# Performance work log

Measured on AMD Instinct MI355X. Metric: run time of the kernel, lower is better.

Reference implementation:

```python
import jax, jax.numpy as jnp
import numpy as np

NUM_HEADS = 16


def setup_inputs() -> dict:
    key = jax.random.key(0)
    k1, k2, k3, k4 = jax.random.split(key, 4)
    B, N, C = 4, 2048, 1024
    x = jax.random.normal(k1, (B, N, C), dtype=jnp.float32)
    # xavier-uniform-ish scaling for stable softmax
    Wqkv = jax.random.normal(k2, (C, 3 * C), dtype=jnp.float32) * (2.0 / (C + 3 * C)) ** 0.5
    Wproj = jax.random.normal(k3, (C, C), dtype=jnp.float32) * (1.0 / C) ** 0.5
    bproj = jnp.zeros((C,), dtype=jnp.float32)
    mask = jax.random.randint(k4, (B, N), 0, 2, dtype=jnp.int32)  # >0 means masked
    return {"x": x, "Wqkv": Wqkv, "Wproj": Wproj, "bproj": bproj, "mask": mask}


def reference(x, Wqkv, Wproj, bproj, mask):
    B, N, C = x.shape
    H = NUM_HEADS
    Dh = C // H
    scale = Dh ** -0.5
    qkv = x @ Wqkv                                   # [B, N, 3C]
    qkv = qkv.reshape(B, N, 3, H, Dh).transpose(2, 0, 3, 1, 4)  # [3, B, H, N, Dh]
    q, k, v = qkv[0], qkv[1], qkv[2]
    att = jnp.einsum('bhqd,bhkd->bhqk', q, k) * scale  # [B, H, N, N]
    att = jnp.where(mask[:, None, None, :] > 0, jnp.float32(-10000000.0), att)
    att = jax.nn.softmax(att, axis=-1)
    out = jnp.einsum('bhqk,bhkd->bhqd', att, v)      # [B, H, N, Dh]
    out = out.transpose(0, 2, 1, 3).reshape(B, N, C)
    return out @ Wproj + bproj
```

## Files before the change

kernel.cpp:

```cpp
#include <hip/hip_runtime.h>
#include <hip/hip_bf16.h>
#include <cstdint>

typedef __bf16 bf16x8 __attribute__((ext_vector_type(8)));
typedef float f32x4 __attribute__((ext_vector_type(4)));
typedef uint4 __attribute__((may_alias)) uint4a;

#define BATCH 4
#define SEQ   2048
#define CDIM  1024
#define NH    16
#define HD    64
#define MROWS (BATCH*SEQ)

__device__ __forceinline__ unsigned short f2bf(float f) {
    uint32_t u = __builtin_bit_cast(uint32_t, f);
    u += 0x7fffu + ((u >> 16) & 1u);
    return (unsigned short)(u >> 16);
}

__global__ void cvt_bf16_kernel(const float* __restrict__ in,
                                unsigned short* __restrict__ out, int n) {
    int i = (blockIdx.x * blockDim.x + threadIdx.x) * 4;
    if (i + 3 < n) {
        float4 v = *(const float4*)(in + i);
        ushort4 o;
        o.x = f2bf(v.x); o.y = f2bf(v.y); o.z = f2bf(v.z); o.w = f2bf(v.w);
        *(ushort4*)(out + i) = o;
    }
}

__global__ void transpose_cvt_kernel(const float* __restrict__ in,
                                     unsigned short* __restrict__ out,
                                     int R, int Cc) {
    __shared__ float tile[32][33];
    int c0 = blockIdx.x * 32, r0 = blockIdx.y * 32;
    int tx = threadIdx.x, ty = threadIdx.y;
    #pragma unroll
    for (int i = 0; i < 32; i += 8)
        tile[ty + i][tx] = in[(size_t)(r0 + ty + i) * Cc + c0 + tx];
    __syncthreads();
    #pragma unroll
    for (int i = 0; i < 32; i += 8)
        out[(size_t)(c0 + ty + i) * R + r0 + tx] = f2bf(tile[tx][ty + i]);
}

__global__ void mask_scan_kernel(const int* __restrict__ mask,
                                 int* __restrict__ pfx, int* __restrict__ cnt) {
    __shared__ int s[256];
    int b = blockIdx.x, t = threadIdx.x;
    int keep[8], lc = 0;
    #pragma unroll
    for (int u = 0; u < 8; ++u) {
        keep[u] = (mask[b * SEQ + t * 8 + u] > 0) ? 0 : 1;
        lc += keep[u];
    }
    s[t] = lc;
    __syncthreads();
    for (int d = 1; d < 256; d <<= 1) {
        int w = (t >= d) ? s[t - d] : 0;
        __syncthreads();
        s[t] += w;
        __syncthreads();
    }
    int pos = s[t] - lc;
    #pragma unroll
    for (int u = 0; u < 8; ++u) {
        int idx = b * SEQ + t * 8 + u;
        pfx[idx] = keep[u] ? pos++ : -1;
    }
    if (t == 255) cnt[b] = s[255];
}

#define BK 64
#define LDA 72

__global__ __launch_bounds__(256, 2)
void gemm_qkv_kernel(const unsigned short* __restrict__ A,
                     const unsigned short* __restrict__ Bt,
                     const int* __restrict__ pfx,
                     unsigned short* __restrict__ Q,
                     unsigned short* __restrict__ Kc,
                     unsigned short* __restrict__ Vct) {
    __shared__ __align__(16) unsigned short sA[128 * LDA];
    __shared__ __align__(16) unsigned short sB[128 * LDA];
    const int Kdim = 1024;
    int m0 = blockIdx.x * 128;
    int n0 = blockIdx.y * 128;
    int tid = threadIdx.x;
    int wave = tid >> 6, lane = tid & 63;
    int wm = (wave >> 1) * 64, wn = (wave & 1) * 64;
    int l15 = lane & 15, quad = lane >> 4;

    f32x4 acc[4][4] = {};

    for (int k0 = 0; k0 < Kdim; k0 += BK) {
        #pragma unroll
        for (int it = 0; it < 4; ++it) {
            int c = tid + it * 256;
            int r = c >> 3, c8 = (c & 7) * 8;
            uint4 va = *(const uint4a*)(A + (size_t)(m0 + r) * Kdim + k0 + c8);
            *(uint4a*)(&sA[r * LDA + c8]) = va;
            uint4 vb = *(const uint4a*)(Bt + (size_t)(n0 + r) * Kdim + k0 + c8);
            *(uint4a*)(&sB[r * LDA + c8]) = vb;
        }
        __syncthreads();
        #pragma unroll
        for (int kk = 0; kk < BK; kk += 32) {
            bf16x8 af[4], bfr[4];
            #pragma unroll
            for (int i = 0; i < 4; ++i) {
                uint4 v = *(const uint4a*)(&sA[(wm + i * 16 + l15) * LDA + kk + quad * 8]);
                af[i] = __builtin_bit_cast(bf16x8, v);
            }
            #pragma unroll
            for (int j = 0; j < 4; ++j) {
                uint4 v = *(const uint4a*)(&sB[(wn + j * 16 + l15) * LDA + kk + quad * 8]);
                bfr[j] = __builtin_bit_cast(bf16x8, v);
            }
            #pragma unroll
            for (int i = 0; i < 4; ++i)
                #pragma unroll
                for (int j = 0; j < 4; ++j)
                    acc[i][j] = __builtin_amdgcn_mfma_f32_16x16x32_bf16(af[i], bfr[j], acc[i][j], 0, 0, 0);
        }
        __syncthreads();
    }

    #pragma unroll
    for (int i = 0; i < 4; ++i) {
        #pragma unroll
        for (int j = 0; j < 4; ++j) {
            int col = n0 + wn + j * 16 + l15;
            int three = col >> 10;
            int h = (col >> 6) & 15;
            int d = col & 63;
            int row0 = m0 + wm + i * 16 + quad * 4;
            int b = row0 >> 11, n = row0 & 2047;
            size_t bh = (size_t)(b * NH + h);
            if (three == 0) {
                #pragma unroll
                for (int r = 0; r < 4; ++r)
                    Q[(bh * SEQ + n + r) * HD + d] = f2bf(acc[i][j][r]);
            } else if (three == 1) {
                #pragma unroll
                for (int r = 0; r < 4; ++r) {
                    int pf = pfx[(b << 11) + n + r];
                    if (pf >= 0) Kc[(bh * SEQ + pf) * HD + d] = f2bf(acc[i][j][r]);
                }
            } else {
                #pragma unroll
                for (int r = 0; r < 4; ++r) {
                    int pf = pfx[(b << 11) + n + r];
                    if (pf >= 0) Vct[(bh * HD + d) * SEQ + pf] = f2bf(acc[i][j][r]);
                }
            }
        }
    }
}

__global__ __launch_bounds__(256, 2)
void gemm_proj_kernel(const unsigned short* __restrict__ A,
                      const unsigned short* __restrict__ Bt,
                      const float* __restrict__ bias,
                      float* __restrict__ Out) {
    __shared__ __align__(16) unsigned short sA[128 * LDA];
    __shared__ __align__(16) unsigned short sB[128 * LDA];
    const int Kdim = 1024;
    int m0 = blockIdx.x * 128;
    int n0 = blockIdx.y * 128;
    int tid = threadIdx.x;
    int wave = tid >> 6, lane = tid & 63;
    int wm = (wave >> 1) * 64, wn = (wave & 1) * 64;
    int l15 = lane & 15, quad = lane >> 4;

    f32x4 acc[4][4] = {};

    for (int k0 = 0; k0 < Kdim; k0 += BK) {
        #pragma unroll
        for (int it = 0; it < 4; ++it) {
            int c = tid + it * 256;
            int r = c >> 3, c8 = (c & 7) * 8;
            uint4 va = *(const uint4a*)(A + (size_t)(m0 + r) * Kdim + k0 + c8);
            *(uint4a*)(&sA[r * LDA + c8]) = va;
            uint4 vb = *(const uint4a*)(Bt + (size_t)(n0 + r) * Kdim + k0 + c8);
            *(uint4a*)(&sB[r * LDA + c8]) = vb;
        }
        __syncthreads();
        #pragma unroll
        for (int kk = 0; kk < BK; kk += 32) {
            bf16x8 af[4], bfr[4];
            #pragma unroll
            for (int i = 0; i < 4; ++i) {
                uint4 v = *(const uint4a*)(&sA[(wm + i * 16 + l15) * LDA + kk + quad * 8]);
                af[i] = __builtin_bit_cast(bf16x8, v);
            }
            #pragma unroll
            for (int j = 0; j < 4; ++j) {
                uint4 v = *(const uint4a*)(&sB[(wn + j * 16 + l15) * LDA + kk + quad * 8]);
                bfr[j] = __builtin_bit_cast(bf16x8, v);
            }
            #pragma unroll
            for (int i = 0; i < 4; ++i)
                #pragma unroll
                for (int j = 0; j < 4; ++j)
                    acc[i][j] = __builtin_amdgcn_mfma_f32_16x16x32_bf16(af[i], bfr[j], acc[i][j], 0, 0, 0);
        }
        __syncthreads();
    }

    #pragma unroll
    for (int i = 0; i < 4; ++i) {
        #pragma unroll
        for (int j = 0; j < 4; ++j) {
            int col = n0 + wn + j * 16 + l15;
            float bv = bias[col];
            #pragma unroll
            for (int r = 0; r < 4; ++r) {
                int row = m0 + wm + i * 16 + quad * 4 + r;
                Out[(size_t)row * CDIM + col] = acc[i][j][r] + bv;
            }
        }
    }
}

#define SPD 72

__global__ __launch_bounds__(256, 4)
void flash_attn_kernel(const unsigned short* __restrict__ Q,
                       const unsigned short* __restrict__ Kg,
                       const unsigned short* __restrict__ Vt,
                       const int* __restrict__ cnt,
                       unsigned short* __restrict__ O) {
    int q0 = blockIdx.x * 128;
    int bh = blockIdx.y;
    int b = bh >> 4, h = bh & 15;
    int tid = threadIdx.x;
    int wave = tid >> 6, lane = tid & 63;
    int l15 = lane & 15, quad = lane >> 4;

    const int kn = cnt[b];

    const size_t head_off = (size_t)bh * SEQ * HD;
    const unsigned short* Qh = Q + head_off;
    const unsigned short* Kh = Kg + head_off;
    const unsigned short* Vh = Vt + head_off;

    __shared__ __align__(16) unsigned short sK [64 * 72];
    __shared__ __align__(16) unsigned short sVt[64 * 72];
    __shared__ __align__(16) unsigned short sP [4][2][16 * SPD];

    bf16x8 qf[2][2];
    #pragma unroll
    for (int mt = 0; mt < 2; ++mt) {
        const unsigned short* qp = Qh + (size_t)(q0 + wave * 32 + mt * 16 + l15) * HD + quad * 8;
        qf[mt][0] = __builtin_bit_cast(bf16x8, *(const uint4a*)(qp));
        qf[mt][1] = __builtin_bit_cast(bf16x8, *(const uint4a*)(qp + 32));
    }

    f32x4 oacc[2][4] = {};
    float lpart[2][4] = {};

    const float C1 = 0.18033688011112042f;

    for (int k0 = 0; k0 < kn; k0 += 64) {
        #pragma unroll
        for (int it = 0; it < 2; ++it) {
            int c = tid + it * 256;
            int r = c >> 3, c8 = (c & 7) * 8;
            *(uint4a*)(&sK[r * 72 + c8])  = *(const uint4a*)(Kh + (size_t)(k0 + r) * HD + c8);
            *(uint4a*)(&sVt[r * 72 + c8]) = *(const uint4a*)(Vh + (size_t)r * SEQ + k0 + c8);
        }
        __syncthreads();

        float madd[4];
        #pragma unroll
        for (int j = 0; j < 4; ++j)
            madd[j] = (k0 + j * 16 + l15 < kn) ? 0.f : -1e30f;

        #pragma unroll
        for (int mt = 0; mt < 2; ++mt) {
            f32x4 s[4] = {};
            #pragma unroll
            for (int j = 0; j < 4; ++j) {
                uint4 v0 = *(const uint4a*)(&sK[(j * 16 + l15) * 72 + quad * 8]);
                uint4 v1 = *(const uint4a*)(&sK[(j * 16 + l15) * 72 + 32 + quad * 8]);
                s[j] = __builtin_amdgcn_mfma_f32_16x16x32_bf16(qf[mt][0], __builtin_bit_cast(bf16x8, v0), s[j], 0, 0, 0);
                s[j] = __builtin_amdgcn_mfma_f32_16x16x32_bf16(qf[mt][1], __builtin_bit_cast(bf16x8, v1), s[j], 0, 0, 0);
            }
            #pragma unroll
            for (int j = 0; j < 4; ++j)
                #pragma unroll
                for (int r = 0; r < 4; ++r) {
                    float p = __builtin_amdgcn_exp2f(fmaf(s[j][r], C1, madd[j]));
                    s[j][r] = p;
                    lpart[mt][r] += p;
                }
            unsigned short* sp = &sP[wave][mt][0];
            #pragma unroll
            for (int j = 0; j < 4; ++j)
                #pragma unroll
                for (int r = 0; r < 4; ++r)
                    sp[(quad * 4 + r) * SPD + j * 16 + l15] = f2bf(s[j][r]);
            #pragma unroll
            for (int kc = 0; kc < 2; ++kc) {
                uint4 av = *(const uint4a*)(&sp[l15 * SPD + kc * 32 + quad * 8]);
                bf16x8 af = __builtin_bit_cast(bf16x8, av);
                #pragma unroll
                for (int jd = 0; jd < 4; ++jd) {
                    uint4 bv = *(const uint4a*)(&sVt[(jd * 16 + l15) * 72 + kc * 32 + quad * 8]);
                    oacc[mt][jd] = __builtin_amdgcn_mfma_f32_16x16x32_bf16(af, __builtin_bit_cast(bf16x8, bv), oacc[mt][jd], 0, 0, 0);
                }
            }
        }
        __syncthreads();
    }

    #pragma unroll
    for (int mt = 0; mt < 2; ++mt)
        #pragma unroll
        for (int r = 0; r < 4; ++r) {
            float v = lpart[mt][r];
            #pragma unroll
            for (int d = 1; d < 16; d <<= 1) v += __shfl_xor(v, d);
            lpart[mt][r] = v;
        }

    #pragma unroll
    for (int mt = 0; mt < 2; ++mt)
        #pragma unroll
        for (int jd = 0; jd < 4; ++jd) {
            int d = jd * 16 + l15;
            #pragma unroll
            for (int r = 0; r < 4; ++r) {
                int qrow = q0 + wave * 32 + mt * 16 + quad * 4 + r;
                float val = oacc[mt][jd][r] / lpart[mt][r];
                O[((size_t)(b * SEQ + qrow)) * CDIM + h * HD + d] = f2bf(val);
            }
        }
}

extern "C" void kernel_launch(void* const* d_in, const int* in_sizes, int n_in,
                              void* d_out, int out_size, void* d_ws, size_t ws_size,
                              hipStream_t stream) {
    const float* x     = (const float*)d_in[0];
    const float* Wqkv  = (const float*)d_in[1];
    const float* Wproj = (const float*)d_in[2];
    const float* bproj = (const float*)d_in[3];
    const int*   mask  = (const int*)d_in[4];
    float* out = (float*)d_out;

    char* ws = (char*)d_ws;
    unsigned short* xb     = (unsigned short*)(ws);
    unsigned short* Wqkvt  = (unsigned short*)(ws + (16u << 20));
    unsigned short* Wprojt = (unsigned short*)(ws + (22u << 20));
    unsigned short* Qb     = (unsigned short*)(ws + (24u << 20));
    unsigned short* Kb     = (unsigned short*)(ws + (40u << 20));
    unsigned short* Vtb    = (unsigned short*)(ws + (56u << 20));
    int*            pfx    = (int*)(ws + (72u << 20));
    int*            cntb   = (int*)(ws + (72u << 20) + (32u << 10));

    cvt_bf16_kernel<<<dim3(8192), dim3(256), 0, stream>>>(x, xb, MROWS * CDIM);
    transpose_cvt_kernel<<<dim3(96, 32), dim3(32, 8), 0, stream>>>(Wqkv, Wqkvt, 1024, 3072);
    transpose_cvt_kernel<<<dim3(32, 32), dim3(32, 8), 0, stream>>>(Wproj, Wprojt, 1024, 1024);
    mask_scan_kernel<<<dim3(4), dim3(256), 0, stream>>>(mask, pfx, cntb);
    gemm_qkv_kernel<<<dim3(64, 24), dim3(256), 0, stream>>>(xb, Wqkvt, pfx, Qb, Kb, Vtb);
    flash_attn_kernel<<<dim3(16, 64), dim3(256), 0, stream>>>(Qb, Kb, Vtb, cntb, xb);
    gemm_proj_kernel<<<dim3(64, 8), dim3(256), 0, stream>>>(xb, Wprojt, bproj, out);
}
```

Measured before the change: 267.2 us.

## Use direct global-to-LDS loads with XOR-swizzled shared layout in GEMMs and attention

Replaces the register-staged global-to-shared tile copies in both GEMM kernels and the flash-attention kernel with global_load_lds 16-byte direct transfers into LDS. The padded LDS rows (stride 72) become unpadded 64-element rows with an XOR swizzle on the 16-byte chunk index, and the fragment reads are adjusted to match. This is meant to cut VGPR pressure and the instruction overhead of the copy path while still avoiding bank conflicts, and it shrinks LDS use. The risk is that this relies on 16-byte global_load_lds support and on the swizzled address mapping being exactly right. The loop is still single-buffered and synchronous, so little load latency gets hidden.

```diff
diff --git a/kernel.cpp b/kernel.cpp
--- a/kernel.cpp
+++ b/kernel.cpp
@@ -5,6 +5,9 @@
 typedef __bf16 bf16x8 __attribute__((ext_vector_type(8)));
 typedef float f32x4 __attribute__((ext_vector_type(4)));
 typedef uint4 __attribute__((may_alias)) uint4a;
+
+typedef __attribute__((address_space(3))) unsigned int   lds_u32;
+typedef __attribute__((address_space(1))) const unsigned int gbl_u32;
 
 #define BATCH 4
 #define SEQ   2048
@@ -17,6 +20,10 @@
     uint32_t u = __builtin_bit_cast(uint32_t, f);
     u += 0x7fffu + ((u >> 16) & 1u);
     return (unsigned short)(u >> 16);
+}
+
+__device__ __forceinline__ void g2l16(const unsigned short* g, unsigned short* l) {
+    __builtin_amdgcn_global_load_lds((gbl_u32*)g, (lds_u32*)l, 16, 0, 0);
 }
 
 __global__ void cvt_bf16_kernel(const float* __restrict__ in,
@@ -73,7 +80,6 @@
 }
 
 #define BK 64
-#define LDA 72
 
 __global__ __launch_bounds__(256, 2)
 void gemm_qkv_kernel(const unsigned short* __restrict__ A,
@@ -82,8 +88,8 @@
                      unsigned short* __restrict__ Q,
                      unsigned short* __restrict__ Kc,
                      unsigned short* __restrict__ Vct) {
-    __shared__ __align__(16) unsigned short sA[128 * LDA];
-    __shared__ __align__(16) unsigned short sB[128 * LDA];
+    __shared__ __align__(16) unsigned short sA[128 * 64];
+    __shared__ __align__(16) unsigned short sB[128 * 64];
     const int Kdim = 1024;
     int m0 = blockIdx.x * 128;
     int n0 = blockIdx.y * 128;
@@ -91,18 +97,17 @@
     int wave = tid >> 6, lane = tid & 63;
     int wm = (wave >> 1) * 64, wn = (wave & 1) * 64;
     int l15 = lane & 15, quad = lane >> 4;
+    int lr = lane >> 3, lc8 = ((lane & 7) ^ lr) * 8;
 
     f32x4 acc[4][4] = {};
 
     for (int k0 = 0; k0 < Kdim; k0 += BK) {
         #pragma unroll
         for (int it = 0; it < 4; ++it) {
-            int c = tid + it * 256;
-            int r = c >> 3, c8 = (c & 7) * 8;
-            uint4 va = *(const uint4a*)(A + (size_t)(m0 + r) * Kdim + k0 + c8);
-            *(uint4a*)(&sA[r * LDA + c8]) = va;
-            uint4 vb = *(const uint4a*)(Bt + (size_t)(n0 + r) * Kdim + k0 + c8);
-            *(uint4a*)(&sB[r * LDA + c8]) = vb;
+            int c = wave * 4 + it;
+            int gr = c * 8 + lr;
+            g2l16(A  + (size_t)(m0 + gr) * Kdim + k0 + lc8, &sA[c * 512]);
+            g2l16(Bt + (size_t)(n0 + gr) * Kdim + k0 + lc8, &sB[c * 512]);
         }
         __syncthreads();
         #pragma unroll
@@ -110,13 +115,15 @@
             bf16x8 af[4], bfr[4];
             #pragma unroll
             for (int i = 0; i < 4; ++i) {
-                uint4 v = *(const uint4a*)(&sA[(wm + i * 16 + l15) * LDA + kk + quad * 8]);
-                af[i] = __builtin_bit_cast(bf16x8, v);
+                int r = wm + i * 16 + l15;
+                int q = ((kk >> 3) + quad) ^ (r & 7);
+                af[i] = __builtin_bit_cast(bf16x8, *(const uint4a*)(&sA[r * 64 + q * 8]));
             }
             #pragma unroll
             for (int j = 0; j < 4; ++j) {
-                uint4 v = *(const uint4a*)(&sB[(wn + j * 16 + l15) * LDA + kk + quad * 8]);
-                bfr[j] = __builtin_bit_cast(bf16x8, v);
+                int r = wn + j * 16 + l15;
+                int q = ((kk >> 3) + quad) ^ (r & 7);
+                bfr[j] = __builtin_bit_cast(bf16x8, *(const uint4a*)(&sB[r * 64 + q * 8]));
             }
             #pragma unroll
             for (int i = 0; i < 4; ++i)
@@ -164,8 +171,8 @@
                       const unsigned short* __restrict__ Bt,
                       const float* __restrict__ bias,
                       float* __restrict__ Out) {
-    __shared__ __align__(16) unsigned short sA[128 * LDA];
-    __shared__ __align__(16) unsigned short sB[128 * LDA];
+    __shared__ __align__(16) unsigned short sA[128 * 64];
+    __shared__ __align__(16) unsigned short sB[128 * 64];
     const int Kdim = 1024;
     int m0 = blockIdx.x * 128;
     int n0 = blockIdx.y * 128;
@@ -173,18 +180,17 @@
     int wave = tid >> 6, lane = tid & 63;
     int wm = (wave >> 1) * 64, wn = (wave & 1) * 64;
     int l15 = lane & 15, quad = lane >> 4;
+    int lr = lane >> 3, lc8 = ((lane & 7) ^ lr) * 8;
 
     f32x4 acc[4][4] = {};
 
     for (int k0 = 0; k0 < Kdim; k0 += BK) {
         #pragma unroll
         for (int it = 0; it < 4; ++it) {
-            int c = tid + it * 256;
-            int r = c >> 3, c8 = (c & 7) * 8;
-            uint4 va = *(const uint4a*)(A + (size_t)(m0 + r) * Kdim + k0 + c8);
-            *(uint4a*)(&sA[r * LDA + c8]) = va;
-            uint4 vb = *(const uint4a*)(Bt + (size_t)(n0 + r) * Kdim + k0 + c8);
-            *(uint4a*)(&sB[r * LDA + c8]) = vb;
+            int c = wave * 4 + it;
+            int gr = c * 8 + lr;
+            g2l16(A  + (size_t)(m0 + gr) * Kdim + k0 + lc8, &sA[c * 512]);
+            g2l16(Bt + (size_t)(n0 + gr) * Kdim + k0 + lc8, &sB[c * 512]);
         }
         __syncthreads();
         #pragma unroll
@@ -192,13 +198,15 @@
             bf16x8 af[4], bfr[4];
             #pragma unroll
             for (int i = 0; i < 4; ++i) {
-                uint4 v = *(const uint4a*)(&sA[(wm + i * 16 + l15) * LDA + kk + quad * 8]);
-                af[i] = __builtin_bit_cast(bf16x8, v);
+                int r = wm + i * 16 + l15;
+                int q = ((kk >> 3) + quad) ^ (r & 7);
+                af[i] = __builtin_bit_cast(bf16x8, *(const uint4a*)(&sA[r * 64 + q * 8]));
             }
             #pragma unroll
             for (int j = 0; j < 4; ++j) {
-                uint4 v = *(const uint4a*)(&sB[(wn + j * 16 + l15) * LDA + kk + quad * 8]);
-                bfr[j] = __builtin_bit_cast(bf16x8, v);
+                int r = wn + j * 16 + l15;
+                int q = ((kk >> 3) + quad) ^ (r & 7);
+                bfr[j] = __builtin_bit_cast(bf16x8, *(const uint4a*)(&sB[r * 64 + q * 8]));
             }
             #pragma unroll
             for (int i = 0; i < 4; ++i)
@@ -238,6 +246,7 @@
     int tid = threadIdx.x;
     int wave = tid >> 6, lane = tid & 63;
     int l15 = lane & 15, quad = lane >> 4;
+    int lr = lane >> 3, lc8 = ((lane & 7) ^ lr) * 8;
 
     const int kn = cnt[b];
 
@@ -246,8 +255,8 @@
     const unsigned short* Kh = Kg + head_off;
     const unsigned short* Vh = Vt + head_off;
 
-    __shared__ __align__(16) unsigned short sK [64 * 72];
-    __shared__ __align__(16) unsigned short sVt[64 * 72];
+    __shared__ __align__(16) unsigned short sK [64 * 64];
+    __shared__ __align__(16) unsigned short sVt[64 * 64];
     __shared__ __align__(16) unsigned short sP [4][2][16 * SPD];
 
     bf16x8 qf[2][2];
@@ -266,10 +275,10 @@
     for (int k0 = 0; k0 < kn; k0 += 64) {
         #pragma unroll
         for (int it = 0; it < 2; ++it) {
-            int c = tid + it * 256;
-            int r = c >> 3, c8 = (c & 7) * 8;
-            *(uint4a*)(&sK[r * 72 + c8])  = *(const uint4a*)(Kh + (size_t)(k0 + r) * HD + c8);
-            *(uint4a*)(&sVt[r * 72 + c8]) = *(const uint4a*)(Vh + (size_t)r * SEQ + k0 + c8);
+            int c = wave * 2 + it;
+            int gr = c * 8 + lr;
+            g2l16(Kh + (size_t)(k0 + gr) * HD + lc8, &sK[c * 512]);
+            g2l16(Vh + (size_t)gr * SEQ + k0 + lc8, &sVt[c * 512]);
         }
         __syncthreads();
 
@@ -283,8 +292,9 @@
             f32x4 s[4] = {};
             #pragma unroll
             for (int j = 0; j < 4; ++j) {
-                uint4 v0 = *(const uint4a*)(&sK[(j * 16 + l15) * 72 + quad * 8]);
-                uint4 v1 = *(const uint4a*)(&sK[(j * 16 + l15) * 72 + 32 + quad * 8]);
+                int r = j * 16 + l15, sw = r & 7;
+                uint4 v0 = *(const uint4a*)(&sK[r * 64 + ((quad ^ sw) * 8)]);
+                uint4 v1 = *(const uint4a*)(&sK[r * 64 + (((4 + quad) ^ sw) * 8)]);
                 s[j] = __builtin_amdgcn_mfma_f32_16x16x32_bf16(qf[mt][0], __builtin_bit_cast(bf16x8, v0), s[j], 0, 0, 0);
                 s[j] = __builtin_amdgcn_mfma_f32_16x16x32_bf16(qf[mt][1], __builtin_bit_cast(bf16x8, v1), s[j], 0, 0, 0);
             }
@@ -308,7 +318,9 @@
                 bf16x8 af = __builtin_bit_cast(bf16x8, av);
                 #pragma unroll
                 for (int jd = 0; jd < 4; ++jd) {
-                    uint4 bv = *(const uint4a*)(&sVt[(jd * 16 + l15) * 72 + kc * 32 + quad * 8]);
+                    int r = jd * 16 + l15;
+                    int q = ((kc * 4 + quad) ^ (r & 7)) * 8;
+                    uint4 bv = *(const uint4a*)(&sVt[r * 64 + q]);
                     oacc[mt][jd] = __builtin_amdgcn_mfma_f32_16x16x32_bf16(af, __builtin_bit_cast(bf16x8, bv), oacc[mt][jd], 0, 0, 0);
                 }
             }
```

Result: faster. 256.0 us (-4.2%).
